# Optimization experiments

Hardware: AMD Instinct MI355X
Metric: run time of the kernel (lower is better)

Reference implementation:

```python
import jax
jax.config.update("jax_enable_x64", True)
import jax.numpy as jnp
import numpy as np

NUM_ENTRIES = 1_000_000
NUM_HINTS = 32_768
MAX_SUBSET = 512
CHUNKS = 5


def setup_inputs() -> dict:
    key = jax.random.key(0)
    k1, k2, k3 = jax.random.split(key, 3)
    entries = jax.random.randint(
        k1, (NUM_ENTRIES, CHUNKS), 0, 2**62, dtype=jnp.int64
    )
    padded_indices = jax.random.randint(
        k2, (NUM_HINTS, MAX_SUBSET), 0, NUM_ENTRIES, dtype=jnp.int64
    )
    valid_mask = jax.random.bernoulli(k3, 0.5, (NUM_HINTS, MAX_SUBSET))
    return {
        "entries": entries,
        "padded_indices": padded_indices,
        "valid_mask": valid_mask,
    }


def reference(entries, padded_indices, valid_mask):
    # gather: [num_hints, max_subset, 5]; invalid slots zeroed (XOR identity)
    gathered = jnp.where(
        valid_mask[:, :, None], entries[padded_indices], jnp.int64(0)
    )
    # XOR-reduce over the subset dimension -> [num_hints, 5]
    parity = jax.lax.reduce(
        gathered, jnp.int64(0), jax.lax.bitwise_xor, (1,)
    )
    return parity
```

## Files before the change

### kernel.cpp

```cpp
#include <hip/hip_runtime.h>
#include <stdint.h>

#define NUM_ENTRIES 1000000
#define NUM_HINTS   32768
#define MAX_SUBSET  512
#define CHUNKS      5

typedef unsigned uint4a4 __attribute__((ext_vector_type(4), aligned(4)));

__global__ __launch_bounds__(256) void hint_xor_kernel(
    const void* __restrict__ entries_v,
    const void* __restrict__ indices_v,
    const void* __restrict__ mask_v,
    int* __restrict__ out)
{
    const int wave = threadIdx.x >> 6;
    const int lane = threadIdx.x & 63;
    const int hint = blockIdx.x * 4 + wave;

    const unsigned* ew = (const unsigned*)entries_v;
    const unsigned* iw = (const unsigned*)indices_v;
    const unsigned* mw = (const unsigned*)mask_v;
    const unsigned es = ew[lane];
    const unsigned is = iw[lane];
    const unsigned ms = mw[lane];
    const bool odd = (lane & 1) != 0;

    const bool ent32  = __any(odd && (es & 0xC0000000u));
    const bool idx32  = __any(odd && (is != 0u));
    const bool m_bytes = __any((ms != 0u) && (ms != 1u) && (ms != 0x3f800000u));
    const bool m_odd_nz = __any(odd && (ms != 0u));
    const int  mstep = m_odd_nz ? 1 : 2;

    const int*            idx32p = (const int*)indices_v;
    const long long*      idx64p = (const long long*)indices_v;
    const unsigned char*  m8p    = (const unsigned char*)mask_v;
    const unsigned*       m32p   = (const unsigned*)mask_v;

    const size_t rowoff = (size_t)hint * MAX_SUBSET;

    unsigned a0 = 0, a1 = 0, a2 = 0, a3 = 0, a4 = 0;

    #pragma unroll
    for (int k = 0; k < 8; ++k) {
        const size_t s = rowoff + (size_t)(k * 64 + lane);

        long long idx;
        if (idx32) idx = (long long)__builtin_nontemporal_load(idx32p + s);
        else       idx = __builtin_nontemporal_load(idx64p + s);

        unsigned mv;
        if (m_bytes) mv = (unsigned)__builtin_nontemporal_load(m8p + s);
        else         mv = __builtin_nontemporal_load(m32p + s * (size_t)mstep);

        const bool v = (mv != 0u) &&
                       ((unsigned long long)idx < (unsigned long long)NUM_ENTRIES);

        if (v) {
            if (ent32) {
                const char* e = (const char*)entries_v + (size_t)idx * 20u;
                const uint4a4 q = *(const uint4a4*)e;
                const unsigned t = *(const unsigned*)(e + 16);
                a0 ^= q.x; a1 ^= q.y; a2 ^= q.z; a3 ^= q.w; a4 ^= t;
            } else {
                const unsigned* e = (const unsigned*)entries_v + (size_t)idx * 10u;
                a0 ^= e[0]; a1 ^= e[2]; a2 ^= e[4]; a3 ^= e[6]; a4 ^= e[8];
            }
        }
    }

    #pragma unroll
    for (int off = 32; off >= 1; off >>= 1) {
        a0 ^= (unsigned)__shfl_xor((int)a0, off, 64);
        a1 ^= (unsigned)__shfl_xor((int)a1, off, 64);
        a2 ^= (unsigned)__shfl_xor((int)a2, off, 64);
        a3 ^= (unsigned)__shfl_xor((int)a3, off, 64);
        a4 ^= (unsigned)__shfl_xor((int)a4, off, 64);
    }

    if (lane < 5) {
        unsigned r = a0;
        r = (lane == 1) ? a1 : r;
        r = (lane == 2) ? a2 : r;
        r = (lane == 3) ? a3 : r;
        r = (lane == 4) ? a4 : r;
        out[(size_t)hint * CHUNKS + lane] = (int)r;
    }
}

extern "C" void kernel_launch(void* const* d_in, const int* in_sizes, int n_in,
                              void* d_out, int out_size, void* d_ws, size_t ws_size,
                              hipStream_t stream) {
    const void* entries = d_in[0];
    const void* indices = d_in[1];
    const void* mask    = d_in[2];
    int*        out     = (int*)d_out;

    hint_xor_kernel<<<NUM_HINTS / 4, 256, 0, stream>>>(entries, indices, mask, out);
}
```

Baseline: 271.2 us.

## Process four hints per wave with sliced entry-table passes for cache locality

Each wave now handles four hints. It loads each lane's eight indices and mask bytes as vector loads up front and packs the mask into a bitmask. The random gathers are then done in eight passes, each touching one slice of the entry table, so that concurrently running waves hit a smaller working set that fits better in L2/MALL. This costs more registers (offsets plus 20 accumulators), repeated predicate checks across the slice passes, and fewer blocks. A fallback generic path handles other input layouts.

```diff
diff --git a/kernel.cpp b/kernel.cpp
--- a/kernel.cpp
+++ b/kernel.cpp
@@ -5,18 +5,24 @@
 #define NUM_HINTS   32768
 #define MAX_SUBSET  512
 #define CHUNKS      5
+#define ROW_BYTES   20
+#define SLICES      8
+#define SLICE_BYTES (NUM_ENTRIES / SLICES * ROW_BYTES)
+#define HPW         4
 
-typedef unsigned uint4a4 __attribute__((ext_vector_type(4), aligned(4)));
+typedef unsigned u32x4a4 __attribute__((ext_vector_type(4), aligned(4)));
+typedef unsigned u32x2a4 __attribute__((ext_vector_type(2), aligned(4)));
 
-__global__ __launch_bounds__(256) void hint_xor_kernel(
+__global__ __launch_bounds__(256, 8) void hint_xor_kernel(
     const void* __restrict__ entries_v,
     const void* __restrict__ indices_v,
     const void* __restrict__ mask_v,
     int* __restrict__ out)
 {
-    const int wave = threadIdx.x >> 6;
-    const int lane = threadIdx.x & 63;
-    const int hint = blockIdx.x * 4 + wave;
+    const int wave  = threadIdx.x >> 6;
+    const int lane  = threadIdx.x & 63;
+    const int gw    = blockIdx.x * 4 + wave;
+    const int hint0 = gw * HPW;
 
     const unsigned* ew = (const unsigned*)entries_v;
     const unsigned* iw = (const unsigned*)indices_v;
@@ -25,66 +31,109 @@
     const unsigned is = iw[lane];
     const unsigned ms = mw[lane];
     const bool odd = (lane & 1) != 0;
-
-    const bool ent32  = __any(odd && (es & 0xC0000000u));
-    const bool idx32  = __any(odd && (is != 0u));
+    const bool ent32   = __any(odd && (es & 0xC0000000u));
+    const bool idx32   = __any(odd && (is != 0u));
     const bool m_bytes = __any((ms != 0u) && (ms != 1u) && (ms != 0x3f800000u));
     const bool m_odd_nz = __any(odd && (ms != 0u));
     const int  mstep = m_odd_nz ? 1 : 2;
 
-    const int*            idx32p = (const int*)indices_v;
-    const long long*      idx64p = (const long long*)indices_v;
-    const unsigned char*  m8p    = (const unsigned char*)mask_v;
-    const unsigned*       m32p   = (const unsigned*)mask_v;
+    unsigned acc[HPW][CHUNKS];
+    #pragma unroll
+    for (int j = 0; j < HPW; ++j)
+        #pragma unroll
+        for (int c = 0; c < CHUNKS; ++c) acc[j][c] = 0u;
 
-    const size_t rowoff = (size_t)hint * MAX_SUBSET;
+    if (ent32 && idx32 && m_bytes) {
+        const int*           idxp  = (const int*)indices_v;
+        const unsigned char* mp    = (const unsigned char*)mask_v;
+        const char*          ebase = (const char*)entries_v;
 
-    unsigned a0 = 0, a1 = 0, a2 = 0, a3 = 0, a4 = 0;
+        unsigned off[HPW][8];
+        unsigned mbits = 0;
+        #pragma unroll
+        for (int j = 0; j < HPW; ++j) {
+            const size_t base = (size_t)(hint0 + j) * MAX_SUBSET + 8u * lane;
+            const u32x4a4 i0 = __builtin_nontemporal_load((const u32x4a4*)(idxp + base));
+            const u32x4a4 i1 = __builtin_nontemporal_load((const u32x4a4*)(idxp + base + 4));
+            off[j][0] = i0.x * 20u; off[j][1] = i0.y * 20u;
+            off[j][2] = i0.z * 20u; off[j][3] = i0.w * 20u;
+            off[j][4] = i1.x * 20u; off[j][5] = i1.y * 20u;
+            off[j][6] = i1.z * 20u; off[j][7] = i1.w * 20u;
+            const u32x2a4 mv = __builtin_nontemporal_load((const u32x2a4*)(mp + base));
+            #pragma unroll
+            for (int k = 0; k < 4; ++k) {
+                if ((mv.x >> (8 * k)) & 0xFFu) mbits |= 1u << (j * 8 + k);
+                if ((mv.y >> (8 * k)) & 0xFFu) mbits |= 1u << (j * 8 + 4 + k);
+            }
+        }
 
-    #pragma unroll
-    for (int k = 0; k < 8; ++k) {
-        const size_t s = rowoff + (size_t)(k * 64 + lane);
+        #pragma unroll 1
+        for (int p = 0; p < SLICES; ++p) {
+            const unsigned lo = (unsigned)p * (unsigned)SLICE_BYTES;
+            #pragma unroll
+            for (int j = 0; j < HPW; ++j) {
+                #pragma unroll
+                for (int k = 0; k < 8; ++k) {
+                    const unsigned o = off[j][k];
+                    const bool hit = ((mbits >> (j * 8 + k)) & 1u) &&
+                                     (o - lo < (unsigned)SLICE_BYTES);
+                    if (hit) {
+                        const u32x4a4 q = *(const u32x4a4*)(ebase + o);
+                        const unsigned t = *(const unsigned*)(ebase + o + 16);
+                        acc[j][0] ^= q.x; acc[j][1] ^= q.y; acc[j][2] ^= q.z;
+                        acc[j][3] ^= q.w; acc[j][4] ^= t;
+                    }
+                }
+            }
+        }
+    } else {
+        const int*           idx32p = (const int*)indices_v;
+        const long long*     idx64p = (const long long*)indices_v;
+        const unsigned char* m8p    = (const unsigned char*)mask_v;
+        const unsigned*      m32p   = (const unsigned*)mask_v;
 
-        long long idx;
-        if (idx32) idx = (long long)__builtin_nontemporal_load(idx32p + s);
-        else       idx = __builtin_nontemporal_load(idx64p + s);
-
-        unsigned mv;
-        if (m_bytes) mv = (unsigned)__builtin_nontemporal_load(m8p + s);
-        else         mv = __builtin_nontemporal_load(m32p + s * (size_t)mstep);
-
-        const bool v = (mv != 0u) &&
-                       ((unsigned long long)idx < (unsigned long long)NUM_ENTRIES);
-
-        if (v) {
-            if (ent32) {
-                const char* e = (const char*)entries_v + (size_t)idx * 20u;
-                const uint4a4 q = *(const uint4a4*)e;
-                const unsigned t = *(const unsigned*)(e + 16);
-                a0 ^= q.x; a1 ^= q.y; a2 ^= q.z; a3 ^= q.w; a4 ^= t;
-            } else {
-                const unsigned* e = (const unsigned*)entries_v + (size_t)idx * 10u;
-                a0 ^= e[0]; a1 ^= e[2]; a2 ^= e[4]; a3 ^= e[6]; a4 ^= e[8];
+        #pragma unroll 1
+        for (int j = 0; j < HPW; ++j) {
+            const size_t rowoff = (size_t)(hint0 + j) * MAX_SUBSET;
+            #pragma unroll 1
+            for (int k = 0; k < 8; ++k) {
+                const size_t s = rowoff + (size_t)(k * 64 + lane);
+                long long idx = idx32 ? (long long)idx32p[s] : idx64p[s];
+                unsigned mv = m_bytes ? (unsigned)m8p[s] : m32p[s * (size_t)mstep];
+                const bool v = (mv != 0u) &&
+                               ((unsigned long long)idx < (unsigned long long)NUM_ENTRIES);
+                if (v) {
+                    if (ent32) {
+                        const unsigned* e = (const unsigned*)entries_v + (size_t)idx * 5u;
+                        acc[j][0] ^= e[0]; acc[j][1] ^= e[1]; acc[j][2] ^= e[2];
+                        acc[j][3] ^= e[3]; acc[j][4] ^= e[4];
+                    } else {
+                        const unsigned* e = (const unsigned*)entries_v + (size_t)idx * 10u;
+                        acc[j][0] ^= e[0]; acc[j][1] ^= e[2]; acc[j][2] ^= e[4];
+                        acc[j][3] ^= e[6]; acc[j][4] ^= e[8];
+                    }
+                }
             }
         }
     }
 
     #pragma unroll
-    for (int off = 32; off >= 1; off >>= 1) {
-        a0 ^= (unsigned)__shfl_xor((int)a0, off, 64);
-        a1 ^= (unsigned)__shfl_xor((int)a1, off, 64);
-        a2 ^= (unsigned)__shfl_xor((int)a2, off, 64);
-        a3 ^= (unsigned)__shfl_xor((int)a3, off, 64);
-        a4 ^= (unsigned)__shfl_xor((int)a4, off, 64);
+    for (int o = 32; o >= 1; o >>= 1) {
+        #pragma unroll
+        for (int j = 0; j < HPW; ++j)
+            #pragma unroll
+            for (int c = 0; c < CHUNKS; ++c)
+                acc[j][c] ^= (unsigned)__shfl_xor((int)acc[j][c], o, 64);
     }
 
-    if (lane < 5) {
-        unsigned r = a0;
-        r = (lane == 1) ? a1 : r;
-        r = (lane == 2) ? a2 : r;
-        r = (lane == 3) ? a3 : r;
-        r = (lane == 4) ? a4 : r;
-        out[(size_t)hint * CHUNKS + lane] = (int)r;
+    if (lane < HPW * CHUNKS) {
+        unsigned v = 0;
+        #pragma unroll
+        for (int j = 0; j < HPW; ++j)
+            #pragma unroll
+            for (int c = 0; c < CHUNKS; ++c)
+                v = (lane == j * CHUNKS + c) ? acc[j][c] : v;
+        out[(size_t)hint0 * CHUNKS + lane] = (int)v;
     }
 }
 
@@ -96,5 +145,5 @@
     const void* mask    = d_in[2];
     int*        out     = (int*)d_out;
 
-    hint_xor_kernel<<<NUM_HINTS / 4, 256, 0, stream>>>(entries, indices, mask, out);
+    hint_xor_kernel<<<NUM_HINTS / (4 * HPW), 256, 0, stream>>>(entries, indices, mask, out);
 }
```

Result: slower. 398.7 us (+47.0%).
